# Optimization experiments

Measured on AMD Instinct MI355X. Metric: run time of the kernel, lower is better.

Reference implementation:

```python
import jax, jax.numpy as jnp
import numpy as np

B = 4096          # batch size
D = 64            # embedding dim
V = 1000000       # num_items
S = 40960         # num_sampled * B = 10 * 4096
NUM_TRIES = 50000 # rejection-sampling tries (deterministic stand-in)


def _sample_unique_log_uniform(rng, num_sampled, num_items):
    """Vectorized stand-in for the torch host-side rejection/dedup loop."""
    ids = np.empty(0, dtype=np.int64)
    while ids.size < num_sampled:
        u = rng.random(num_sampled * 4)
        cand = (np.floor(np.exp(u * np.log(num_items + 1.0))).astype(np.int64) - 1) % num_items
        both = np.concatenate([ids, cand])
        _, first = np.unique(both, return_index=True)
        ids = both[np.sort(first)]  # unique, first-occurrence order
    return ids[:num_sampled]


def setup_inputs() -> dict:
    key = jax.random.key(0)
    k1, k2, k3 = jax.random.split(key, 3)
    rng = np.random.default_rng(0)
    sampled = jnp.asarray(_sample_unique_log_uniform(rng, S, V), dtype=jnp.int64)
    return {
        "user_embeddings": jax.random.normal(k1, (B, D), jnp.float32),
        "item_embeddings": jax.random.normal(k2, (V, D), jnp.float32) * 0.05,
        "item_bias": jnp.zeros((V,), jnp.float32),
        "positive_item_ids": jax.random.randint(k3, (B,), 0, V, dtype=jnp.int64),
        "sampled_item_ids": sampled,
        "num_tries": NUM_TRIES,
    }


def _log_uniform_prob(ids, num_items):
    f = ids.astype(jnp.float32)
    return (jnp.log(f + 2.0) - jnp.log(f + 1.0)) / jnp.log(jnp.float32(num_items + 1))


def _expected_counts(p, num_tries):
    tiny = jnp.float32(np.finfo(np.float32).tiny)
    return jnp.maximum(1.0 - jnp.power(1.0 - p, jnp.float32(num_tries)), tiny)


def reference(user_embeddings, item_embeddings, item_bias, positive_item_ids, sampled_item_ids, num_tries):
    num_items = item_embeddings.shape[0]
    # positive logits [B,1]
    pos_emb = item_embeddings[positive_item_ids]                      # [B,D]
    pos_logits = jnp.sum(user_embeddings * pos_emb, axis=-1, keepdims=True) \
                 + item_bias[positive_item_ids][:, None]
    # sampled logits [B,S]
    samp_emb = item_embeddings[sampled_item_ids]                      # [S,D]
    samp_logits = user_embeddings @ samp_emb.T + item_bias[sampled_item_ids][None, :]
    # mask accidental hits
    hits = positive_item_ids[:, None] == sampled_item_ids[None, :]    # [B,S]
    samp_logits = jnp.where(hits, jnp.float32(-np.finfo(np.float32).max), samp_logits)
    # sampled-softmax expected-count correction
    pos_exp = _expected_counts(_log_uniform_prob(positive_item_ids, num_items), num_tries)
    samp_exp = _expected_counts(_log_uniform_prob(sampled_item_ids, num_items), num_tries)
    pos_logits = pos_logits - jnp.log(pos_exp)[:, None]
    samp_logits = samp_logits - jnp.log(samp_exp)[None, :]
    # cross-entropy with label 0 (the positive column)
    logits = jnp.concatenate([pos_logits, samp_logits], axis=1)       # [B,1+S]
    loss = jnp.mean(jax.nn.logsumexp(logits, axis=-1) - logits[:, 0])
    return loss
```

## Files before the change

kernel.cpp:

```cpp
#include <hip/hip_runtime.h>
#include <math.h>

typedef __attribute__((ext_vector_type(8))) short bf16x8;
typedef __attribute__((ext_vector_type(4))) float f32x4;
typedef __attribute__((ext_vector_type(4))) int i32x4;
typedef __attribute__((ext_vector_type(4))) unsigned short u16x4;

#define LOG2E 1.4426950408889634f
#define LN2   0.6931471805599453f
#define FTINY 1.1754943508222875e-38f
#define MOFF  16.0f

constexpr int Dd = 64;
constexpr int Bb = 4096;
constexpr int Ss = 40960;
constexpr int BN = 256;
constexpr int SCHUNK = 64;
constexpr int STILES = 32;
constexpr int SPB = Ss / STILES;
constexpr int NCHUNK = SPB / SCHUNK;

constexpr int SAMP_BLOCKS = Ss / 16;
constexpr int FILL_BLOCKS = 977;
constexpr int USER_BLOCKS = (Bb * Dd / 4) / 256;
constexpr int C2_BLOCKS   = Ss / 256;

static __device__ __forceinline__ unsigned short f2bf(float x) {
    unsigned int u = __float_as_uint(x);
    u += 0x7fffu + ((u >> 16) & 1u);
    return (unsigned short)(u >> 16);
}

static __device__ __forceinline__ float neg_log_expected(int id, float invLogV1, float T) {
    float f = (float)id;
    float p = log1pf(1.0f / (f + 1.0f)) * invLogV1;
    float pw = powf(1.0f - p, T);
    float se = fmaxf(1.0f - pw, FTINY);
    return -logf(se);
}

__global__ void k_prep(const float* __restrict__ user, const float* __restrict__ item,
                       const float* __restrict__ bias, const int* __restrict__ sampled,
                       const int* __restrict__ ntries,
                       unsigned short* __restrict__ Ebf, unsigned short* __restrict__ Ubf,
                       float* __restrict__ c2, int* __restrict__ tbl,
                       unsigned int* __restrict__ cnt, float invLogV1, int V) {
    const int bid = blockIdx.x, tid = threadIdx.x;
    if (bid < SAMP_BLOCKS) {
        const int ri = tid >> 4, c = tid & 15;
        const int s = bid * 16 + ri;
        const int sid = sampled[s];
        f32x4 v = *(const f32x4*)(item + (size_t)sid * Dd + c * 4);
        u16x4 o;
        o[0] = f2bf(v[0]); o[1] = f2bf(v[1]); o[2] = f2bf(v[2]); o[3] = f2bf(v[3]);
        *(u16x4*)(Ebf + (size_t)s * Dd + c * 4) = o;
    } else if (bid < SAMP_BLOCKS + FILL_BLOCKS) {
        const int fb = bid - SAMP_BLOCKS;
        if (fb == 0 && tid == 0) *cnt = 0u;
        const int base = (fb * 256 + tid) * 4;
        if (base + 3 < V) {
            i32x4 m1 = {-1, -1, -1, -1};
            *(i32x4*)(tbl + base) = m1;
        } else {
            for (int i = base; i < V; ++i) tbl[i] = -1;
        }
    } else if (bid < SAMP_BLOCKS + FILL_BLOCKS + USER_BLOCKS) {
        const int i = (bid - SAMP_BLOCKS - FILL_BLOCKS) * 256 + tid;
        f32x4 v = *(const f32x4*)(user + (size_t)i * 4);
        u16x4 o;
        o[0] = f2bf(v[0] * LOG2E); o[1] = f2bf(v[1] * LOG2E);
        o[2] = f2bf(v[2] * LOG2E); o[3] = f2bf(v[3] * LOG2E);
        *(u16x4*)(Ubf + (size_t)i * 4) = o;
    } else {
        const int s = (bid - SAMP_BLOCKS - FILL_BLOCKS - USER_BLOCKS) * 256 + tid;
        const int sid = sampled[s];
        const float T = (float)ntries[0];
        c2[s] = (bias[sid] + neg_log_expected(sid, invLogV1, T)) * LOG2E - MOFF;
    }
}

__global__ __launch_bounds__(256) void ssl_main(
    const unsigned short* __restrict__ Ebf, const unsigned short* __restrict__ Ubf,
    const float* __restrict__ c2, const int* __restrict__ sampled,
    int* __restrict__ tbl, float* __restrict__ partials)
{
    __shared__ __align__(16) unsigned short lds[SCHUNK * Dd];
    const int tid = threadIdx.x;
    const int w = tid >> 6, l = tid & 63;
    const int g16 = l >> 4, l16 = l & 15;
    const int stile = blockIdx.x, btile = blockIdx.y;

    const int fid = blockIdx.x + STILES * blockIdx.y;
    if (fid < Ss / 256) {
        const int s = fid * 256 + tid;
        tbl[sampled[s]] = s;
    }

    const int s0 = stile * SPB;
    const int colb = btile * BN + w * 64;
    bf16x8 bf[4][2];
    #pragma unroll
    for (int g = 0; g < 4; ++g) {
        const unsigned short* up = Ubf + (size_t)(colb + g * 16 + l16) * Dd + g16 * 8;
        bf[g][0] = *(const bf16x8*)(up);
        bf[g][1] = *(const bf16x8*)(up + 32);
    }

    float rl0 = 0.f, rl1 = 0.f, rl2 = 0.f, rl3 = 0.f;

    const int srow = tid >> 3, scs = tid & 7;
    const int csrc = scs ^ (srow & 7);
    const unsigned short* stgp = Ebf + (size_t)(s0 + srow) * Dd + csrc * 8;
    bf16x8 stg0 = *(const bf16x8*)stgp;
    bf16x8 stg1 = *(const bf16x8*)(stgp + 32 * Dd);
    const float* c2b = c2 + s0 + g16 * 4;

    for (int ch = 0; ch < NCHUNK; ++ch) {
        __syncthreads();
        *(bf16x8*)(lds + tid * 8) = stg0;
        *(bf16x8*)(lds + tid * 8 + 32 * Dd) = stg1;
        if (ch + 1 < NCHUNK) {
            stg0 = *(const bf16x8*)(stgp + (size_t)(ch + 1) * SCHUNK * Dd);
            stg1 = *(const bf16x8*)(stgp + (size_t)(ch + 1) * SCHUNK * Dd + 32 * Dd);
        }
        const float* c2c = c2b + ch * SCHUNK;
        f32x4 cc0 = *(const f32x4*)(c2c);
        f32x4 cc1 = *(const f32x4*)(c2c + 16);
        f32x4 cc2 = *(const f32x4*)(c2c + 32);
        f32x4 cc3 = *(const f32x4*)(c2c + 48);
        __syncthreads();

        #pragma unroll
        for (int t = 0; t < 4; ++t) {
            const int r = t * 16 + l16;
            const int sw = r & 7;
            const bf16x8 a0 = *(const bf16x8*)(lds + r * Dd + (((g16    ) ^ sw) << 3));
            const bf16x8 a1 = *(const bf16x8*)(lds + r * Dd + (((g16 + 4) ^ sw) << 3));
            const f32x4 cc = (t == 0) ? cc0 : (t == 1) ? cc1 : (t == 2) ? cc2 : cc3;
            #pragma unroll
            for (int g = 0; g < 4; ++g) {
                f32x4 acc = cc;
                acc = __builtin_amdgcn_mfma_f32_16x16x32_bf16(a0, bf[g][0], acc, 0, 0, 0);
                acc = __builtin_amdgcn_mfma_f32_16x16x32_bf16(a1, bf[g][1], acc, 0, 0, 0);
                float e = (__builtin_amdgcn_exp2f(acc[0]) + __builtin_amdgcn_exp2f(acc[1]))
                        + (__builtin_amdgcn_exp2f(acc[2]) + __builtin_amdgcn_exp2f(acc[3]));
                if      (g == 0) rl0 += e;
                else if (g == 1) rl1 += e;
                else if (g == 2) rl2 += e;
                else             rl3 += e;
            }
        }
    }

    rl0 += __shfl_xor(rl0, 16); rl0 += __shfl_xor(rl0, 32);
    rl1 += __shfl_xor(rl1, 16); rl1 += __shfl_xor(rl1, 32);
    rl2 += __shfl_xor(rl2, 16); rl2 += __shfl_xor(rl2, 32);
    rl3 += __shfl_xor(rl3, 16); rl3 += __shfl_xor(rl3, 32);
    if (l < 16) {
        partials[(size_t)(colb +  0 + l16) * STILES + stile] = rl0;
        partials[(size_t)(colb + 16 + l16) * STILES + stile] = rl1;
        partials[(size_t)(colb + 32 + l16) * STILES + stile] = rl2;
        partials[(size_t)(colb + 48 + l16) * STILES + stile] = rl3;
    }
}

__global__ void k_final(const float* __restrict__ user, const float* __restrict__ item,
                        const float* __restrict__ bias, const int* __restrict__ posids,
                        const int* __restrict__ ntries, const float* __restrict__ partials,
                        const float* __restrict__ c2, const int* __restrict__ tbl,
                        float* __restrict__ bsums, unsigned int* __restrict__ cnt,
                        float* __restrict__ out, float invLogV1) {
    const int tid = threadIdx.x, sub = tid & 3;
    const int b = blockIdx.x * 64 + (tid >> 2);
    const int pid = posids[b];
    const float T = (float)ntries[0];
    const f32x4* up = (const f32x4*)(user + (size_t)b * Dd + sub * 16);
    const f32x4* ep = (const f32x4*)(item + (size_t)pid * Dd + sub * 16);
    f32x4 dv = {0.f, 0.f, 0.f, 0.f};
    #pragma unroll
    for (int i = 0; i < 4; ++i) {
        f32x4 uu = up[i], ee = ep[i];
        dv[0] = fmaf(uu[0], ee[0], dv[0]); dv[1] = fmaf(uu[1], ee[1], dv[1]);
        dv[2] = fmaf(uu[2], ee[2], dv[2]); dv[3] = fmaf(uu[3], ee[3], dv[3]);
    }
    float d = (dv[0] + dv[1]) + (dv[2] + dv[3]);
    d += __shfl_xor(d, 1); d += __shfl_xor(d, 2);
    const float* pp = partials + (size_t)b * STILES + sub * 8;
    f32x4 p0 = *(const f32x4*)pp, p1 = *(const f32x4*)(pp + 4);
    float S = ((p0[0] + p0[1]) + (p0[2] + p0[3])) + ((p1[0] + p1[1]) + (p1[2] + p1[3]));
    S += __shfl_xor(S, 1); S += __shfl_xor(S, 2);

    const float pb2 = (d + bias[pid] + neg_log_expected(pid, invLogV1, T)) * LOG2E;
    const int sh = tbl[pid];
    if (sh >= 0) S -= __builtin_amdgcn_exp2f(fmaf(d, LOG2E, c2[sh]));
    S += __builtin_amdgcn_exp2f(pb2 - MOFF);
    float loss = (MOFF + log2f(S) - pb2) * LN2;

    #pragma unroll
    for (int off = 1; off < 64; off <<= 1) loss += __shfl_xor(loss, off);
    __shared__ float wsum[4];
    if ((tid & 63) == 0) wsum[tid >> 6] = loss;
    __syncthreads();
    if (tid == 0) {
        bsums[blockIdx.x] = wsum[0] + wsum[1] + wsum[2] + wsum[3];
        __threadfence();
        if (atomicAdd(cnt, 1u) == 63u) {
            __threadfence();
            float tot = 0.f;
            for (int i = 0; i < 64; ++i) tot += bsums[i];
            out[0] = tot * (1.0f / (4.0f * (float)Bb));
        }
    }
}

extern "C" void kernel_launch(void* const* d_in, const int* in_sizes, int n_in,
                              void* d_out, int out_size, void* d_ws, size_t ws_size,
                              hipStream_t stream) {
    (void)n_in; (void)out_size; (void)ws_size;
    const float* user    = (const float*)d_in[0];
    const float* item    = (const float*)d_in[1];
    const float* bias    = (const float*)d_in[2];
    const int*   posids  = (const int*)d_in[3];
    const int*   sampled = (const int*)d_in[4];
    const int*   ntries  = (const int*)d_in[5];
    float* out = (float*)d_out;

    const int V = in_sizes[2];
    const float invLogV1 = 1.0f / logf((float)V + 1.0f);

    char* p = (char*)d_ws;
    auto alloc = [&](size_t bytes) {
        char* r = p;
        p += (bytes + 255) & ~(size_t)255;
        return r;
    };
    unsigned short* Ebf     = (unsigned short*)alloc((size_t)Ss * Dd * 2);
    unsigned short* Ubf     = (unsigned short*)alloc((size_t)Bb * Dd * 2);
    float*          c2      = (float*)alloc((size_t)Ss * 4);
    float*          partial = (float*)alloc((size_t)Bb * STILES * 4);
    int*            tbl     = (int*)alloc((size_t)V * 4);
    float*          bsums   = (float*)alloc(64 * 4);
    unsigned int*   cnt     = (unsigned int*)alloc(256);

    k_prep<<<SAMP_BLOCKS + FILL_BLOCKS + USER_BLOCKS + C2_BLOCKS, 256, 0, stream>>>(
        user, item, bias, sampled, ntries, Ebf, Ubf, c2, tbl, cnt, invLogV1, V);
    ssl_main<<<dim3(STILES, Bb / BN), 256, 0, stream>>>(Ebf, Ubf, c2, sampled, tbl, partial);
    k_final<<<Bb / 64, 256, 0, stream>>>(user, item, bias, posids, ntries,
                                         partial, c2, tbl, bsums, cnt, out, invLogV1);
}
```

Measured before the change: 52.39 us.

## Replace hit lookup table with bitmap and fuse final reduction into main kernel

The 4 MB per-item index table, which had to be filled with -1 on every call, is replaced by a roughly 125 KB bitmap of sampled ids. Each main-kernel block sets its share of bits with atomicOr. The separate final kernel is removed: the last block to finish each batch tile waits on a counter for all bitmap updates, then reduces the partials and computes the per-row loss. Positive logits move into the prep kernel, the user bf16 conversion moves into the main kernel, and the LDS chunk grows to 128 rows. For accidental hits, the positive term is now skipped instead of subtracting the bf16 sampled logit, which changes rounding slightly. The spin-wait relies on every block being resident or progressing.

```diff
diff --git a/kernel.cpp b/kernel.cpp
--- a/kernel.cpp
+++ b/kernel.cpp
@@ -15,15 +15,15 @@
 constexpr int Bb = 4096;
 constexpr int Ss = 40960;
 constexpr int BN = 256;
-constexpr int SCHUNK = 64;
+constexpr int SCHUNK = 128;
 constexpr int STILES = 32;
 constexpr int SPB = Ss / STILES;
 constexpr int NCHUNK = SPB / SCHUNK;
-
-constexpr int SAMP_BLOCKS = Ss / 16;
-constexpr int FILL_BLOCKS = 977;
-constexpr int USER_BLOCKS = (Bb * Dd / 4) / 256;
-constexpr int C2_BLOCKS   = Ss / 256;
+constexpr int NBLOCKS = STILES * (Bb / BN);
+
+constexpr int GATHER_BLOCKS = Ss / 16;
+constexpr int C2_BLOCKS = Ss / 256;
+constexpr int POS_BLOCKS = Bb / 64;
 
 static __device__ __forceinline__ unsigned short f2bf(float x) {
     unsigned int u = __float_as_uint(x);
@@ -41,12 +41,12 @@
 
 __global__ void k_prep(const float* __restrict__ user, const float* __restrict__ item,
                        const float* __restrict__ bias, const int* __restrict__ sampled,
-                       const int* __restrict__ ntries,
-                       unsigned short* __restrict__ Ebf, unsigned short* __restrict__ Ubf,
-                       float* __restrict__ c2, int* __restrict__ tbl,
-                       unsigned int* __restrict__ cnt, float invLogV1, int V) {
+                       const int* __restrict__ posids, const int* __restrict__ ntries,
+                       unsigned short* __restrict__ Ebf, float* __restrict__ c2,
+                       float* __restrict__ pos2, unsigned int* __restrict__ bm,
+                       unsigned int* __restrict__ ctr, float invLogV1, int nbmw, int zb) {
     const int bid = blockIdx.x, tid = threadIdx.x;
-    if (bid < SAMP_BLOCKS) {
+    if (bid < GATHER_BLOCKS) {
         const int ri = tid >> 4, c = tid & 15;
         const int s = bid * 16 + ri;
         const int sid = sampled[s];
@@ -54,56 +54,87 @@
         u16x4 o;
         o[0] = f2bf(v[0]); o[1] = f2bf(v[1]); o[2] = f2bf(v[2]); o[3] = f2bf(v[3]);
         *(u16x4*)(Ebf + (size_t)s * Dd + c * 4) = o;
-    } else if (bid < SAMP_BLOCKS + FILL_BLOCKS) {
-        const int fb = bid - SAMP_BLOCKS;
-        if (fb == 0 && tid == 0) *cnt = 0u;
-        const int base = (fb * 256 + tid) * 4;
-        if (base + 3 < V) {
-            i32x4 m1 = {-1, -1, -1, -1};
-            *(i32x4*)(tbl + base) = m1;
+    } else if (bid < GATHER_BLOCKS + zb) {
+        const int z = bid - GATHER_BLOCKS;
+        const int base = (z * 256 + tid) * 4;
+        if (base + 3 < nbmw) {
+            i32x4 zz = {0, 0, 0, 0};
+            *(i32x4*)((int*)bm + base) = zz;
         } else {
-            for (int i = base; i < V; ++i) tbl[i] = -1;
-        }
-    } else if (bid < SAMP_BLOCKS + FILL_BLOCKS + USER_BLOCKS) {
-        const int i = (bid - SAMP_BLOCKS - FILL_BLOCKS) * 256 + tid;
-        f32x4 v = *(const f32x4*)(user + (size_t)i * 4);
-        u16x4 o;
-        o[0] = f2bf(v[0] * LOG2E); o[1] = f2bf(v[1] * LOG2E);
-        o[2] = f2bf(v[2] * LOG2E); o[3] = f2bf(v[3] * LOG2E);
-        *(u16x4*)(Ubf + (size_t)i * 4) = o;
-    } else {
-        const int s = (bid - SAMP_BLOCKS - FILL_BLOCKS - USER_BLOCKS) * 256 + tid;
+            for (int i = base; i < nbmw; ++i) bm[i] = 0u;
+        }
+        if (z == 0 && tid < 18) ctr[tid] = 0u;
+    } else if (bid < GATHER_BLOCKS + zb + C2_BLOCKS) {
+        const int s = (bid - GATHER_BLOCKS - zb) * 256 + tid;
         const int sid = sampled[s];
         const float T = (float)ntries[0];
         c2[s] = (bias[sid] + neg_log_expected(sid, invLogV1, T)) * LOG2E - MOFF;
+    } else {
+        const int pbk = bid - GATHER_BLOCKS - zb - C2_BLOCKS;
+        const int sub = tid & 3, b = pbk * 64 + (tid >> 2);
+        const int pid = posids[b];
+        const f32x4* up = (const f32x4*)(user + (size_t)b * Dd + sub * 16);
+        const f32x4* ep = (const f32x4*)(item + (size_t)pid * Dd + sub * 16);
+        f32x4 dv = {0.f, 0.f, 0.f, 0.f};
+        #pragma unroll
+        for (int i = 0; i < 4; ++i) {
+            f32x4 uu = up[i], ee = ep[i];
+            dv[0] = fmaf(uu[0], ee[0], dv[0]); dv[1] = fmaf(uu[1], ee[1], dv[1]);
+            dv[2] = fmaf(uu[2], ee[2], dv[2]); dv[3] = fmaf(uu[3], ee[3], dv[3]);
+        }
+        float d = (dv[0] + dv[1]) + (dv[2] + dv[3]);
+        d += __shfl_xor(d, 1); d += __shfl_xor(d, 2);
+        if (sub == 0) {
+            const float T = (float)ntries[0];
+            pos2[b] = (d + bias[pid] + neg_log_expected(pid, invLogV1, T)) * LOG2E;
+        }
     }
 }
 
 __global__ __launch_bounds__(256) void ssl_main(
-    const unsigned short* __restrict__ Ebf, const unsigned short* __restrict__ Ubf,
+    const unsigned short* __restrict__ Ebf, const float* __restrict__ user,
     const float* __restrict__ c2, const int* __restrict__ sampled,
-    int* __restrict__ tbl, float* __restrict__ partials)
+    const int* __restrict__ posids, const float* __restrict__ pos2,
+    unsigned int* __restrict__ bm, unsigned int* __restrict__ ctr,
+    float* __restrict__ partials, float* __restrict__ bsums, float* __restrict__ out)
 {
     __shared__ __align__(16) unsigned short lds[SCHUNK * Dd];
+    __shared__ float redbuf[4];
+    __shared__ unsigned int fin_flag;
     const int tid = threadIdx.x;
     const int w = tid >> 6, l = tid & 63;
     const int g16 = l >> 4, l16 = l & 15;
     const int stile = blockIdx.x, btile = blockIdx.y;
-
-    const int fid = blockIdx.x + STILES * blockIdx.y;
-    if (fid < Ss / 256) {
-        const int s = fid * 256 + tid;
-        tbl[sampled[s]] = s;
-    }
+    const int fid = stile + STILES * btile;
+
+    if (tid < 80) {
+        const int sid = sampled[fid * 80 + tid];
+        atomicOr(&bm[sid >> 5], 1u << (sid & 31));
+    }
+    __syncthreads();
+    if (tid == 0) { __threadfence(); atomicAdd(&ctr[0], 1u); }
 
     const int s0 = stile * SPB;
     const int colb = btile * BN + w * 64;
+
     bf16x8 bf[4][2];
     #pragma unroll
     for (int g = 0; g < 4; ++g) {
-        const unsigned short* up = Ubf + (size_t)(colb + g * 16 + l16) * Dd + g16 * 8;
-        bf[g][0] = *(const bf16x8*)(up);
-        bf[g][1] = *(const bf16x8*)(up + 32);
+        const float* up = user + (size_t)(colb + g * 16 + l16) * Dd + g16 * 8;
+        f32x4 u0 = *(const f32x4*)(up);
+        f32x4 u1 = *(const f32x4*)(up + 4);
+        f32x4 u2 = *(const f32x4*)(up + 32);
+        f32x4 u3 = *(const f32x4*)(up + 36);
+        bf16x8 f0, f1;
+        f0[0] = (short)f2bf(u0[0] * LOG2E); f0[1] = (short)f2bf(u0[1] * LOG2E);
+        f0[2] = (short)f2bf(u0[2] * LOG2E); f0[3] = (short)f2bf(u0[3] * LOG2E);
+        f0[4] = (short)f2bf(u1[0] * LOG2E); f0[5] = (short)f2bf(u1[1] * LOG2E);
+        f0[6] = (short)f2bf(u1[2] * LOG2E); f0[7] = (short)f2bf(u1[3] * LOG2E);
+        f1[0] = (short)f2bf(u2[0] * LOG2E); f1[1] = (short)f2bf(u2[1] * LOG2E);
+        f1[2] = (short)f2bf(u2[2] * LOG2E); f1[3] = (short)f2bf(u2[3] * LOG2E);
+        f1[4] = (short)f2bf(u3[0] * LOG2E); f1[5] = (short)f2bf(u3[1] * LOG2E);
+        f1[6] = (short)f2bf(u3[2] * LOG2E); f1[7] = (short)f2bf(u3[3] * LOG2E);
+        bf[g][0] = f0; bf[g][1] = f1;
     }
 
     float rl0 = 0.f, rl1 = 0.f, rl2 = 0.f, rl3 = 0.f;
@@ -111,43 +142,58 @@
     const int srow = tid >> 3, scs = tid & 7;
     const int csrc = scs ^ (srow & 7);
     const unsigned short* stgp = Ebf + (size_t)(s0 + srow) * Dd + csrc * 8;
-    bf16x8 stg0 = *(const bf16x8*)stgp;
+    bf16x8 stg0 = *(const bf16x8*)(stgp);
     bf16x8 stg1 = *(const bf16x8*)(stgp + 32 * Dd);
+    bf16x8 stg2 = *(const bf16x8*)(stgp + 64 * Dd);
+    bf16x8 stg3 = *(const bf16x8*)(stgp + 96 * Dd);
     const float* c2b = c2 + s0 + g16 * 4;
 
     for (int ch = 0; ch < NCHUNK; ++ch) {
         __syncthreads();
-        *(bf16x8*)(lds + tid * 8) = stg0;
-        *(bf16x8*)(lds + tid * 8 + 32 * Dd) = stg1;
+        *(bf16x8*)(lds + tid * 8)            = stg0;
+        *(bf16x8*)(lds + tid * 8 + 32 * Dd)  = stg1;
+        *(bf16x8*)(lds + tid * 8 + 64 * Dd)  = stg2;
+        *(bf16x8*)(lds + tid * 8 + 96 * Dd)  = stg3;
         if (ch + 1 < NCHUNK) {
-            stg0 = *(const bf16x8*)(stgp + (size_t)(ch + 1) * SCHUNK * Dd);
-            stg1 = *(const bf16x8*)(stgp + (size_t)(ch + 1) * SCHUNK * Dd + 32 * Dd);
-        }
+            const unsigned short* np = stgp + (size_t)(ch + 1) * SCHUNK * Dd;
+            stg0 = *(const bf16x8*)(np);
+            stg1 = *(const bf16x8*)(np + 32 * Dd);
+            stg2 = *(const bf16x8*)(np + 64 * Dd);
+            stg3 = *(const bf16x8*)(np + 96 * Dd);
+        }
+        __syncthreads();
+
         const float* c2c = c2b + ch * SCHUNK;
-        f32x4 cc0 = *(const f32x4*)(c2c);
-        f32x4 cc1 = *(const f32x4*)(c2c + 16);
-        f32x4 cc2 = *(const f32x4*)(c2c + 32);
-        f32x4 cc3 = *(const f32x4*)(c2c + 48);
-        __syncthreads();
-
         #pragma unroll
-        for (int t = 0; t < 4; ++t) {
+        for (int t = 0; t < 8; ++t) {
             const int r = t * 16 + l16;
             const int sw = r & 7;
             const bf16x8 a0 = *(const bf16x8*)(lds + r * Dd + (((g16    ) ^ sw) << 3));
             const bf16x8 a1 = *(const bf16x8*)(lds + r * Dd + (((g16 + 4) ^ sw) << 3));
-            const f32x4 cc = (t == 0) ? cc0 : (t == 1) ? cc1 : (t == 2) ? cc2 : cc3;
-            #pragma unroll
-            for (int g = 0; g < 4; ++g) {
-                f32x4 acc = cc;
-                acc = __builtin_amdgcn_mfma_f32_16x16x32_bf16(a0, bf[g][0], acc, 0, 0, 0);
-                acc = __builtin_amdgcn_mfma_f32_16x16x32_bf16(a1, bf[g][1], acc, 0, 0, 0);
-                float e = (__builtin_amdgcn_exp2f(acc[0]) + __builtin_amdgcn_exp2f(acc[1]))
-                        + (__builtin_amdgcn_exp2f(acc[2]) + __builtin_amdgcn_exp2f(acc[3]));
-                if      (g == 0) rl0 += e;
-                else if (g == 1) rl1 += e;
-                else if (g == 2) rl2 += e;
-                else             rl3 += e;
+            const f32x4 cc = *(const f32x4*)(c2c + t * 16);
+            {
+                f32x4 acc = __builtin_amdgcn_mfma_f32_16x16x32_bf16(a0, bf[0][0], cc, 0, 0, 0);
+                acc = __builtin_amdgcn_mfma_f32_16x16x32_bf16(a1, bf[0][1], acc, 0, 0, 0);
+                rl0 += (__builtin_amdgcn_exp2f(acc[0]) + __builtin_amdgcn_exp2f(acc[1]))
+                     + (__builtin_amdgcn_exp2f(acc[2]) + __builtin_amdgcn_exp2f(acc[3]));
+            }
+            {
+                f32x4 acc = __builtin_amdgcn_mfma_f32_16x16x32_bf16(a0, bf[1][0], cc, 0, 0, 0);
+                acc = __builtin_amdgcn_mfma_f32_16x16x32_bf16(a1, bf[1][1], acc, 0, 0, 0);
+                rl1 += (__builtin_amdgcn_exp2f(acc[0]) + __builtin_amdgcn_exp2f(acc[1]))
+                     + (__builtin_amdgcn_exp2f(acc[2]) + __builtin_amdgcn_exp2f(acc[3]));
+            }
+            {
+                f32x4 acc = __builtin_amdgcn_mfma_f32_16x16x32_bf16(a0, bf[2][0], cc, 0, 0, 0);
+                acc = __builtin_amdgcn_mfma_f32_16x16x32_bf16(a1, bf[2][1], acc, 0, 0, 0);
+                rl2 += (__builtin_amdgcn_exp2f(acc[0]) + __builtin_amdgcn_exp2f(acc[1]))
+                     + (__builtin_amdgcn_exp2f(acc[2]) + __builtin_amdgcn_exp2f(acc[3]));
+            }
+            {
+                f32x4 acc = __builtin_amdgcn_mfma_f32_16x16x32_bf16(a0, bf[3][0], cc, 0, 0, 0);
+                acc = __builtin_amdgcn_mfma_f32_16x16x32_bf16(a1, bf[3][1], acc, 0, 0, 0);
+                rl3 += (__builtin_amdgcn_exp2f(acc[0]) + __builtin_amdgcn_exp2f(acc[1]))
+                     + (__builtin_amdgcn_exp2f(acc[2]) + __builtin_amdgcn_exp2f(acc[3]));
             }
         }
     }
@@ -162,53 +208,46 @@
         partials[(size_t)(colb + 32 + l16) * STILES + stile] = rl2;
         partials[(size_t)(colb + 48 + l16) * STILES + stile] = rl3;
     }
-}
-
-__global__ void k_final(const float* __restrict__ user, const float* __restrict__ item,
-                        const float* __restrict__ bias, const int* __restrict__ posids,
-                        const int* __restrict__ ntries, const float* __restrict__ partials,
-                        const float* __restrict__ c2, const int* __restrict__ tbl,
-                        float* __restrict__ bsums, unsigned int* __restrict__ cnt,
-                        float* __restrict__ out, float invLogV1) {
-    const int tid = threadIdx.x, sub = tid & 3;
-    const int b = blockIdx.x * 64 + (tid >> 2);
-    const int pid = posids[b];
-    const float T = (float)ntries[0];
-    const f32x4* up = (const f32x4*)(user + (size_t)b * Dd + sub * 16);
-    const f32x4* ep = (const f32x4*)(item + (size_t)pid * Dd + sub * 16);
-    f32x4 dv = {0.f, 0.f, 0.f, 0.f};
+
+    if (tid == 0) {
+        __threadfence();
+        unsigned int old = atomicAdd(&ctr[1 + btile], 1u);
+        fin_flag = (old == (unsigned)(STILES - 1)) ? 1u : 0u;
+    }
+    __syncthreads();
+    if (fin_flag == 0u) return;
+
+    if (tid == 0) {
+        while (atomicAdd(&ctr[0], 0u) < (unsigned)NBLOCKS) __builtin_amdgcn_s_sleep(2);
+    }
+    __syncthreads();
+
+    const int col = btile * BN + tid;
+    const float* pp = partials + (size_t)col * STILES;
+    float S = 0.f;
     #pragma unroll
-    for (int i = 0; i < 4; ++i) {
-        f32x4 uu = up[i], ee = ep[i];
-        dv[0] = fmaf(uu[0], ee[0], dv[0]); dv[1] = fmaf(uu[1], ee[1], dv[1]);
-        dv[2] = fmaf(uu[2], ee[2], dv[2]); dv[3] = fmaf(uu[3], ee[3], dv[3]);
-    }
-    float d = (dv[0] + dv[1]) + (dv[2] + dv[3]);
-    d += __shfl_xor(d, 1); d += __shfl_xor(d, 2);
-    const float* pp = partials + (size_t)b * STILES + sub * 8;
-    f32x4 p0 = *(const f32x4*)pp, p1 = *(const f32x4*)(pp + 4);
-    float S = ((p0[0] + p0[1]) + (p0[2] + p0[3])) + ((p1[0] + p1[1]) + (p1[2] + p1[3]));
-    S += __shfl_xor(S, 1); S += __shfl_xor(S, 2);
-
-    const float pb2 = (d + bias[pid] + neg_log_expected(pid, invLogV1, T)) * LOG2E;
-    const int sh = tbl[pid];
-    if (sh >= 0) S -= __builtin_amdgcn_exp2f(fmaf(d, LOG2E, c2[sh]));
-    S += __builtin_amdgcn_exp2f(pb2 - MOFF);
+    for (int i = 0; i < 8; ++i) {
+        f32x4 p = *(const f32x4*)(pp + i * 4);
+        S += ((p[0] + p[1]) + (p[2] + p[3]));
+    }
+    const float pb2 = pos2[col];
+    const int pid = posids[col];
+    const bool hit = (bm[pid >> 5] >> (pid & 31)) & 1u;
+    if (!hit) S += __builtin_amdgcn_exp2f(pb2 - MOFF);
     float loss = (MOFF + log2f(S) - pb2) * LN2;
 
     #pragma unroll
     for (int off = 1; off < 64; off <<= 1) loss += __shfl_xor(loss, off);
-    __shared__ float wsum[4];
-    if ((tid & 63) == 0) wsum[tid >> 6] = loss;
+    if (l == 0) redbuf[w] = loss;
     __syncthreads();
     if (tid == 0) {
-        bsums[blockIdx.x] = wsum[0] + wsum[1] + wsum[2] + wsum[3];
+        bsums[btile] = (redbuf[0] + redbuf[1]) + (redbuf[2] + redbuf[3]);
         __threadfence();
-        if (atomicAdd(cnt, 1u) == 63u) {
+        if (atomicAdd(&ctr[17], 1u) == (unsigned)(Bb / BN - 1)) {
             __threadfence();
             float tot = 0.f;
-            for (int i = 0; i < 64; ++i) tot += bsums[i];
-            out[0] = tot * (1.0f / (4.0f * (float)Bb));
+            for (int i = 0; i < Bb / BN; ++i) tot += bsums[i];
+            out[0] = tot / (float)Bb;
         }
     }
 }
@@ -227,6 +266,8 @@
 
     const int V = in_sizes[2];
     const float invLogV1 = 1.0f / logf((float)V + 1.0f);
+    const int nbmw = (V + 31) / 32;
+    const int zb = (nbmw + 1023) / 1024;
 
     char* p = (char*)d_ws;
     auto alloc = [&](size_t bytes) {
@@ -235,16 +276,16 @@
         return r;
     };
     unsigned short* Ebf     = (unsigned short*)alloc((size_t)Ss * Dd * 2);
-    unsigned short* Ubf     = (unsigned short*)alloc((size_t)Bb * Dd * 2);
     float*          c2      = (float*)alloc((size_t)Ss * 4);
+    float*          pos2    = (float*)alloc((size_t)Bb * 4);
     float*          partial = (float*)alloc((size_t)Bb * STILES * 4);
-    int*            tbl     = (int*)alloc((size_t)V * 4);
+    unsigned int*   bm      = (unsigned int*)alloc((size_t)nbmw * 4);
     float*          bsums   = (float*)alloc(64 * 4);
-    unsigned int*   cnt     = (unsigned int*)alloc(256);
-
-    k_prep<<<SAMP_BLOCKS + FILL_BLOCKS + USER_BLOCKS + C2_BLOCKS, 256, 0, stream>>>(
-        user, item, bias, sampled, ntries, Ebf, Ubf, c2, tbl, cnt, invLogV1, V);
-    ssl_main<<<dim3(STILES, Bb / BN), 256, 0, stream>>>(Ebf, Ubf, c2, sampled, tbl, partial);
-    k_final<<<Bb / 64, 256, 0, stream>>>(user, item, bias, posids, ntries,
-                                         partial, c2, tbl, bsums, cnt, out, invLogV1);
-}
+    unsigned int*   ctr     = (unsigned int*)alloc(256);
+
+    k_prep<<<GATHER_BLOCKS + zb + C2_BLOCKS + POS_BLOCKS, 256, 0, stream>>>(
+        user, item, bias, sampled, posids, ntries, Ebf, c2, pos2, bm, ctr,
+        invLogV1, nbmw, zb);
+    ssl_main<<<dim3(STILES, Bb / BN), 256, 0, stream>>>(
+        Ebf, user, c2, sampled, posids, pos2, bm, ctr, partial, bsums, out);
+}
```

After: 77.66 us. 48.2% more time.
